# Performance work log

Measured on AMD Instinct MI355X. Metric: run time of the kernel, lower is better.

## Reference

```python
import jax, jax.numpy as jnp
import numpy as np

L, H, D, HS = 6, 8, 512, 64
EPS = 1e-5


def _ln(x, g, b):
    m = jnp.mean(x, -1, keepdims=True)
    v = jnp.mean((x - m) ** 2, -1, keepdims=True)
    return (x - m) * jax.lax.rsqrt(v + EPS) * g + b


def _posenc(T, C):
    pos = jnp.arange(T, dtype=jnp.float32)[:, None]
    div = jnp.exp(jnp.arange(0, C, 2, dtype=jnp.float32) * (-jnp.log(10000.0) / C))
    pe = jnp.zeros((T, C), jnp.float32)
    pe = pe.at[:, 0::2].set(jnp.sin(pos * div))
    pe = pe.at[:, 1::2].set(jnp.cos(pos * div))
    return pe


def setup_inputs() -> dict:
    B, T, F, V, E, O = 8, 1024, 32, 7, 16, 49
    key = jax.random.key(0)
    ks = jax.random.split(key, 16)
    s = 0.02
    inp = {
        'code': jax.random.randint(ks[0], (B, T, F), 0, V),
        'lengths': jax.random.randint(ks[1], (B,), T // 2, T + 1),
        'emb': s * jax.random.normal(ks[2], (V, E), jnp.float32),
        'Wq': s * jax.random.normal(ks[3], (L, H, D, HS), jnp.float32),
        'Wk': s * jax.random.normal(ks[4], (L, H, D, HS), jnp.float32),
        'Wv': s * jax.random.normal(ks[5], (L, H, D, HS), jnp.float32),
        'Wo': s * jax.random.normal(ks[6], (L, D, D), jnp.float32),
        'bo': jnp.zeros((L, D), jnp.float32),
        'W1': s * jax.random.normal(ks[7], (L, D, 4 * D), jnp.float32),
        'b1': jnp.zeros((L, 4 * D), jnp.float32),
        'W2': s * jax.random.normal(ks[8], (L, 4 * D, D), jnp.float32),
        'b2': jnp.zeros((L, D), jnp.float32),
        'ln1_g': jnp.ones((L, D), jnp.float32),
        'ln1_b': jnp.zeros((L, D), jnp.float32),
        'ln2_g': jnp.ones((L, D), jnp.float32),
        'ln2_b': jnp.zeros((L, D), jnp.float32),
        'lnf_g': jnp.ones((D,), jnp.float32),
        'lnf_b': jnp.zeros((D,), jnp.float32),
        'attn_w': s * jax.random.normal(ks[9], (D, 1), jnp.float32),
        'attn_b': jnp.zeros((1,), jnp.float32),
        'head_w': s * jax.random.normal(ks[10], (D, 49), jnp.float32),
        'head_b': jnp.zeros((49,), jnp.float32),
    }
    return inp


def reference(code, lengths, emb, Wq, Wk, Wv, Wo, bo, W1, b1, W2, b2,
              ln1_g, ln1_b, ln2_g, ln2_b, lnf_g, lnf_b,
              attn_w, attn_b, head_w, head_b):
    B, T, F = code.shape
    # token embedding (B,T,F,E) -> (B,T,D) plus sinusoidal positions
    x = emb[code].reshape(B, T, D) + _posenc(T, D)
    mask = jnp.arange(T) < lengths[:, None]          # (B,T) valid positions
    col_mask = mask[:, None, None, :]                # mask key columns
    row_mask = mask[:, None, :, None]                # zero padded query rows
    for l in range(L):
        xn = _ln(x, ln1_g[l], ln1_b[l])
        q = jnp.einsum('btd,hde->bhte', xn, Wq[l])
        k = jnp.einsum('btd,hde->bhte', xn, Wk[l])
        v = jnp.einsum('btd,hde->bhte', xn, Wv[l])
        wei = jnp.einsum('bhte,bhse->bhts', q, k) * (HS ** -0.5)
        wei = jnp.where(col_mask, wei, -jnp.inf)
        wei = jax.nn.softmax(wei, axis=-1)
        wei = jnp.where(row_mask, wei, 0.0)
        o = jnp.einsum('bhts,bhse->bthe', wei, v).reshape(B, T, H * HS)
        x = x + o @ Wo[l] + bo[l]
        xn = _ln(x, ln2_g[l], ln2_b[l])
        x = x + jax.nn.gelu(xn @ W1[l] + b1[l], approximate=False) @ W2[l] + b2[l]
    x = _ln(x, lnf_g, lnf_b)
    # attention pooling over time
    scores = x @ attn_w + attn_b                     # (B,T,1)
    scores = jnp.where(mask[:, :, None], scores, -jnp.inf)
    aw = jax.nn.softmax(scores, axis=1)
    summary = jnp.sum(aw * x, axis=1)                # (B,D)
    logits = summary @ head_w + head_b               # (B,49)
    return logits
```

## Files before the change

### kernel.cpp

```cpp
#include <hip/hip_runtime.h>
#include <math.h>

#define TT 1024
#define BB 8
#define DD 512
#define HH 8
#define HSZ 64
#define LL 6
#define FF4 2048

typedef __attribute__((ext_vector_type(8))) short short8;
typedef __attribute__((ext_vector_type(4))) float floatx4;
typedef unsigned short ushort_t;
typedef unsigned int uint_t;

__device__ __forceinline__ ushort_t f2bf(float f) {
  uint_t u = __float_as_uint(f);
  u += 0x7fff + ((u >> 16) & 1);
  return (ushort_t)(u >> 16);
}
__device__ __forceinline__ float bf2f(ushort_t h) {
  return __uint_as_float(((uint_t)h) << 16);
}

#if defined(__has_builtin)
#if __has_builtin(__builtin_amdgcn_sched_group_barrier)
#define SGB(mask, n) __builtin_amdgcn_sched_group_barrier(mask, n, 0)
#endif
#endif
#ifndef SGB
#define SGB(mask, n)
#endif


__global__ __launch_bounds__(256) void k_embed(const int* __restrict__ code,
                                               const float* __restrict__ emb,
                                               float* __restrict__ x,
                                               const int* __restrict__ lengths) {
  int idx = blockIdx.x * 256 + threadIdx.x;
  int c = idx & (DD - 1);
  int bt = idx >> 9;
  int t = bt & (TT - 1);
  if (t >= lengths[bt >> 10]) return;
  int f = c >> 4, e = c & 15;
  int vv = code[bt * 32 + f];
  int i = c >> 1;
  float freq = expf((float)(2 * i) * (-9.210340371976184f / 512.f));
  float ang = (float)t * freq;
  float pe = (c & 1) ? cosf(ang) : sinf(ang);
  x[idx] = emb[vv * 16 + e] + pe;
}

__global__ __launch_bounds__(256) void k_ln(const float* __restrict__ x,
                                            ushort_t* __restrict__ yB,
                                            float* __restrict__ yF,
                                            const float* __restrict__ g,
                                            const float* __restrict__ b,
                                            const float* __restrict__ aw,
                                            const float* __restrict__ ab,
                                            float* __restrict__ scores,
                                            const int* __restrict__ lengths) {
  int row0 = blockIdx.x * 4;
  if ((row0 & (TT - 1)) >= lengths[row0 >> 10]) return;
  int wave = threadIdx.x >> 6, lane = threadIdx.x & 63;
  int row = row0 + wave;
  const float* xr = x + (size_t)row * DD;
  float v[8];
  *(float4*)&v[0] = *(const float4*)(xr + lane * 8);
  *(float4*)&v[4] = *(const float4*)(xr + lane * 8 + 4);
  float s = 0.f;
#pragma unroll
  for (int j = 0; j < 8; ++j) s += v[j];
#pragma unroll
  for (int off = 32; off; off >>= 1) s += __shfl_down(s, off, 64);
  float mean = __shfl(s, 0, 64) * (1.f / DD);
  float qv = 0.f;
#pragma unroll
  for (int j = 0; j < 8; ++j) { float d = v[j] - mean; qv += d * d; }
#pragma unroll
  for (int off = 32; off; off >>= 1) qv += __shfl_down(qv, off, 64);
  float rs = rsqrtf(__shfl(qv, 0, 64) * (1.f / DD) + 1e-5f);
  float ov[8];
  float sdot = 0.f;
#pragma unroll
  for (int e = 0; e < 8; ++e) {
    int c = lane * 8 + e;
    ov[e] = (v[e] - mean) * rs * g[c] + b[c];
    if (scores) sdot += ov[e] * aw[c];
  }
  if (yB) {
    short8 o8;
#pragma unroll
    for (int e = 0; e < 8; ++e) o8[e] = (short)f2bf(ov[e]);
    size_t ad = (((size_t)(row >> 4) * 16 + (lane >> 2)) << 9) + ((lane & 3) * 16 + (row & 15)) * 8;
    *(short8*)(yB + ad) = o8;
  } else {
    float* yr = yF + (size_t)row * DD + lane * 8;
    *(float4*)yr = *(float4*)&ov[0];
    *(float4*)(yr + 4) = *(float4*)&ov[4];
  }
  if (scores) {
#pragma unroll
    for (int off = 32; off; off >>= 1) sdot += __shfl_down(sdot, off, 64);
    if (lane == 0) scores[row] = sdot + ab[0];
  }
}

__global__ __launch_bounds__(256) void k_packw(const float* __restrict__ in,
                                               ushort_t* __restrict__ out,
                                               int Nin, long in_ms, int nh,
                                               long os_l, int nblk, int Kout) {
  __shared__ float t4[64][65];
  int mz = blockIdx.z;
  const float* ip = in + (size_t)mz * in_ms;
  ushort_t* op = out + (size_t)(mz / nh) * os_l;
  int nbase = (mz % nh) * nblk + blockIdx.y * 64;
  int k0 = blockIdx.x * 64;
  int cc = threadIdx.x & 63, r0 = threadIdx.x >> 6;
#pragma unroll
  for (int i = 0; i < 16; ++i) {
    int r = r0 * 16 + i;
    t4[r][cc] = ip[(size_t)(k0 + r) * Nin + (nbase - (mz % nh) * nblk) + cc];
  }
  __syncthreads();
#pragma unroll
  for (int half = 0; half < 2; ++half) {
    int c = threadIdx.x + half * 256;
    int joct = c >> 6, nl = c & 63;
    int n = nbase + nl, k = k0 + joct * 8;
    short8 v8;
#pragma unroll
    for (int e = 0; e < 8; ++e) v8[e] = (short)f2bf(t4[joct * 8 + e][nl]);
    size_t ad = (((size_t)(n >> 4) * (Kout >> 5) + (k >> 5)) << 9) + (((k >> 3) & 3) * 16 + (n & 15)) * 8;
    *(short8*)(op + ad) = v8;
  }
}

template <int MT, int NT, int D>
__global__ __launch_bounds__(64, (MT == 4) ? 3 : 4) void k_pgemm(const ushort_t* __restrict__ Apk,
                                                                 const ushort_t* __restrict__ Bpk,
                                                                 const float* __restrict__ resid,
                                                                 const float* __restrict__ bias,
                                                                 float* __restrict__ outF,
                                                                 ushort_t* __restrict__ outB,
                                                                 int M, int N, int K, int mode,
                                                                 const int* __restrict__ lengths) {
  __shared__ ushort_t Cb[MT == 4 ? 64 * 80 : 64];
  const int lane = threadIdx.x;
  const int quad = lane >> 4, l16 = lane & 15;
  const int gx = N / (NT * 16);
  int id = blockIdx.x;
  int bx = (id >> 3) % gx;
  int by = (id / (8 * gx)) * 8 + (id & 7);
  const int row0 = by * (MT * 16), col0 = bx * (NT * 16);
  if (lengths && (row0 & (TT - 1)) >= lengths[row0 >> 10]) return;
  const int nk = K >> 5;
  const ushort_t* Ab = Apk + (((size_t)(row0 >> 4) * nk) << 9) + lane * 8;
  const ushort_t* Bb = Bpk + (((size_t)(col0 >> 4) * nk) << 9) + lane * 8;
  floatx4 acc[MT][NT] = {};
  short8 af[D][MT], bf[D][NT];
#pragma unroll
  for (int d = 0; d < D; ++d) {
#pragma unroll
    for (int mt = 0; mt < MT; ++mt) af[d][mt] = *(const short8*)(Ab + (((size_t)(mt * nk + d)) << 9));
#pragma unroll
    for (int nt = 0; nt < NT; ++nt) bf[d][nt] = *(const short8*)(Bb + (((size_t)(nt * nk + d)) << 9));
  }
  int kc = 0;
  for (; kc + D < nk; kc += D) {
#pragma unroll
    for (int d = 0; d < D; ++d) {
#pragma unroll
      for (int mt = 0; mt < MT; ++mt)
#pragma unroll
        for (int nt = 0; nt < NT; ++nt)
          acc[mt][nt] = __builtin_amdgcn_mfma_f32_16x16x32_bf16(af[d][mt], bf[d][nt], acc[mt][nt], 0, 0, 0);
      SGB(0x008, MT * NT);
      const int nxt = kc + d + D;
#pragma unroll
      for (int mt = 0; mt < MT; ++mt) af[d][mt] = *(const short8*)(Ab + (((size_t)(mt * nk + nxt)) << 9));
#pragma unroll
      for (int nt = 0; nt < NT; ++nt) bf[d][nt] = *(const short8*)(Bb + (((size_t)(nt * nk + nxt)) << 9));
      SGB(0x020, MT + NT);
    }
  }
#pragma unroll
  for (int d = 0; d < D; ++d)
#pragma unroll
    for (int mt = 0; mt < MT; ++mt)
#pragma unroll
      for (int nt = 0; nt < NT; ++nt)
        acc[mt][nt] = __builtin_amdgcn_mfma_f32_16x16x32_bf16(af[d][mt], bf[d][nt], acc[mt][nt], 0, 0, 0);

  if (MT == 4 && mode == 2) {
#pragma unroll
    for (int mt = 0; mt < MT; ++mt)
#pragma unroll
      for (int nt = 0; nt < NT; ++nt) {
        floatx4 a4 = acc[mt][nt];
#pragma unroll
        for (int r = 0; r < 4; ++r) {
          float val = a4[r] + bias[col0 + nt * 16 + l16];
          val = 0.5f * val * (1.f + erff(val * 0.7071067811865475f));
          Cb[(mt * 16 + quad * 4 + r) * 80 + nt * 16 + l16] = f2bf(val);
        }
      }
#pragma unroll
    for (int mt2 = 0; mt2 < 4; ++mt2)
#pragma unroll
      for (int kt2 = 0; kt2 < 2; ++kt2) {
        short8 v8 = *(const short8*)&Cb[(mt2 * 16 + l16) * 80 + kt2 * 32 + quad * 8];
        size_t ad = ((((size_t)(row0 >> 4) + mt2) * (N >> 5) + (col0 >> 5) + kt2) << 9) + lane * 8;
        *(short8*)(outB + ad) = v8;
      }
  } else {
    const float qscale = (mode == 3 && col0 < 512) ? 0.125f : 1.0f;
#pragma unroll
    for (int mt = 0; mt < MT; ++mt)
#pragma unroll
      for (int nt = 0; nt < NT; ++nt) {
        floatx4 a4 = acc[mt][nt];
#pragma unroll
        for (int r = 0; r < 4; ++r) {
          int row = row0 + mt * 16 + quad * 4 + r;
          int col = col0 + nt * 16 + l16;
          float val = a4[r];
          if (bias) val += bias[col];
          size_t idx = (size_t)row * N + col;
          if (mode == 1) outF[idx] = val + resid[idx];
          else outB[idx] = f2bf(val * qscale);
        }
      }
  }
}

__global__ __launch_bounds__(256) void k_attn(const ushort_t* __restrict__ qkv,
                                              const int* __restrict__ lengths,
                                              ushort_t* __restrict__ o) {
  __shared__ ushort_t Ks[64 * 72];
  __shared__ ushort_t Vt[64 * 72];
  __shared__ ushort_t Ps[4][16 * 72];
  const int tid = threadIdx.x;
  const int w = tid >> 6, lane = tid & 63;
  const int quad = lane >> 4, l16 = lane & 15;
  const int tile = blockIdx.x & 15;
  const int bh = blockIdx.x >> 4;
  const int b = bh >> 3, h = bh & 7;
  const int len = lengths[b];
  if (tile * 64 >= len) return;
  const int tqa = tile * 64 + w * 16 + l16;
  const ushort_t* qp = qkv + ((size_t)(b * TT + tqa)) * 1536 + h * HSZ + quad * 8;
  short8 qf0 = *(const short8*)qp;
  short8 qf1 = *(const short8*)(qp + 32);
  floatx4 oacc[4] = {};
  float lsum[4] = {0.f, 0.f, 0.f, 0.f};
  const int skey = tid >> 2, sseg = (tid & 3) << 4;
  const int vkp = (tid & 31) << 1, vds = (tid >> 5) << 3;
  const int nkt = (len + 63) >> 6;
  for (int kt = 0; kt < nkt; ++kt) {
    const int s0 = kt * 64;
    __syncthreads();
    {
      const ushort_t* kp = qkv + ((size_t)(b * TT + s0 + skey)) * 1536 + 512 + h * HSZ + sseg;
      short8 k0 = *(const short8*)kp;
      short8 k1 = *(const short8*)(kp + 8);
      *(short8*)&Ks[skey * 72 + sseg] = k0;
      *(short8*)&Ks[skey * 72 + sseg + 8] = k1;
      const ushort_t* vp0 = qkv + ((size_t)(b * TT + s0 + vkp)) * 1536 + 1024 + h * HSZ + vds;
      short8 v0 = *(const short8*)vp0;
      short8 v1 = *(const short8*)(vp0 + 1536);
#pragma unroll
      for (int i = 0; i < 8; ++i) {
        ushort2 pr;
        pr.x = (ushort_t)v0[i];
        pr.y = (ushort_t)v1[i];
        *(ushort2*)&Vt[(vds + i) * 72 + vkp] = pr;
      }
    }
    __syncthreads();
    floatx4 sacc[4] = {};
#pragma unroll
    for (int nt = 0; nt < 4; ++nt) {
      short8 kf0 = *(const short8*)&Ks[(nt * 16 + l16) * 72 + quad * 8];
      short8 kf1 = *(const short8*)&Ks[(nt * 16 + l16) * 72 + 32 + quad * 8];
      sacc[nt] = __builtin_amdgcn_mfma_f32_16x16x32_bf16(qf0, kf0, sacc[nt], 0, 0, 0);
      sacc[nt] = __builtin_amdgcn_mfma_f32_16x16x32_bf16(qf1, kf1, sacc[nt], 0, 0, 0);
    }
    float p[4][4];
    if (kt == nkt - 1) {
#pragma unroll
      for (int nt = 0; nt < 4; ++nt) {
        bool valid = (s0 + nt * 16 + l16 < len);
#pragma unroll
        for (int r = 0; r < 4; ++r) p[nt][r] = valid ? __expf(sacc[nt][r]) : 0.f;
      }
    } else {
#pragma unroll
      for (int nt = 0; nt < 4; ++nt)
#pragma unroll
        for (int r = 0; r < 4; ++r) p[nt][r] = __expf(sacc[nt][r]);
    }
#pragma unroll
    for (int r = 0; r < 4; ++r)
#pragma unroll
      for (int nt = 0; nt < 4; ++nt) {
        lsum[r] += p[nt][r];
        Ps[w][(quad * 4 + r) * 72 + nt * 16 + l16] = f2bf(p[nt][r]);
      }
    short8 pf0 = *(const short8*)&Ps[w][l16 * 72 + quad * 8];
    short8 pf1 = *(const short8*)&Ps[w][l16 * 72 + 32 + quad * 8];
#pragma unroll
    for (int nt = 0; nt < 4; ++nt) {
      short8 vf0 = *(const short8*)&Vt[(nt * 16 + l16) * 72 + quad * 8];
      short8 vf1 = *(const short8*)&Vt[(nt * 16 + l16) * 72 + 32 + quad * 8];
      oacc[nt] = __builtin_amdgcn_mfma_f32_16x16x32_bf16(pf0, vf0, oacc[nt], 0, 0, 0);
      oacc[nt] = __builtin_amdgcn_mfma_f32_16x16x32_bf16(pf1, vf1, oacc[nt], 0, 0, 0);
    }
  }
#pragma unroll
  for (int off = 1; off < 16; off <<= 1) {
#pragma unroll
    for (int r = 0; r < 4; ++r) lsum[r] += __shfl_xor(lsum[r], off, 64);
  }
#pragma unroll
  for (int r = 0; r < 4; ++r) {
    int t = tile * 64 + w * 16 + quad * 4 + r;
    float inv = (t < len) ? 1.f / lsum[r] : 0.f;
#pragma unroll
    for (int nt = 0; nt < 4; ++nt)
      Ps[w][(quad * 4 + r) * 72 + nt * 16 + l16] = f2bf(oacc[nt][r] * inv);
  }
  const int mtile = b * 64 + tile * 4 + w;
#pragma unroll
  for (int kt2 = 0; kt2 < 2; ++kt2) {
    short8 v8 = *(const short8*)&Ps[w][l16 * 72 + kt2 * 32 + quad * 8];
    size_t ad = (((size_t)mtile * 16 + h * 2 + kt2) << 9) + lane * 8;
    *(short8*)(o + ad) = v8;
  }
}

__global__ __launch_bounds__(256) void k_softw(const float* __restrict__ scores,
                                               const int* __restrict__ lengths,
                                               float* __restrict__ wts) {
  __shared__ float red[8];
  int tid = threadIdx.x, b = blockIdx.x;
  int len = lengths[b];
  const float* sb = scores + b * TT;
  float m = -1e30f;
  for (int t = tid; t < len; t += 256) m = fmaxf(m, sb[t]);
#pragma unroll
  for (int off = 32; off; off >>= 1) m = fmaxf(m, __shfl_down(m, off, 64));
  if ((tid & 63) == 0) red[tid >> 6] = m;
  __syncthreads();
  m = fmaxf(fmaxf(red[0], red[1]), fmaxf(red[2], red[3]));
  float ssum = 0.f;
  for (int t = tid; t < len; t += 256) ssum += __expf(sb[t] - m);
#pragma unroll
  for (int off = 32; off; off >>= 1) ssum += __shfl_down(ssum, off, 64);
  if ((tid & 63) == 0) red[4 + (tid >> 6)] = ssum;
  __syncthreads();
  float inv = 1.f / (red[4] + red[5] + red[6] + red[7]);
  for (int t = tid; t < TT; t += 256)
    wts[b * TT + t] = (t < len) ? __expf(sb[t] - m) * inv : 0.f;
}

__global__ __launch_bounds__(256) void k_wsum(const float* __restrict__ xf,
                                              const float* __restrict__ wts,
                                              float* __restrict__ partial,
                                              const int* __restrict__ lengths) {
  int b = blockIdx.x, c = blockIdx.y, tid = threadIdx.x;
  float* pp = partial + ((size_t)b * 16 + c) * DD;
  if (c * 64 >= lengths[b]) {
    pp[tid] = 0.f;
    pp[tid + 256] = 0.f;
    return;
  }
  const float* xb = xf + ((size_t)b * TT + c * 64) * DD;
  const float* wb = wts + b * TT + c * 64;
  float a0 = 0.f, a1 = 0.f;
  for (int t = 0; t < 64; ++t) {
    float wv = wb[t];
    a0 += wv * xb[(size_t)t * DD + tid];
    a1 += wv * xb[(size_t)t * DD + tid + 256];
  }
  pp[tid] = a0;
  pp[tid + 256] = a1;
}

__global__ __launch_bounds__(64) void k_head(const float* __restrict__ partial,
                                             const float* __restrict__ head_w,
                                             const float* __restrict__ head_b,
                                             float* __restrict__ out) {
  __shared__ float ssum[DD];
  int b = blockIdx.x, tid = threadIdx.x;
  for (int d = tid; d < DD; d += 64) {
    float s = 0.f;
#pragma unroll
    for (int c = 0; c < 16; ++c) s += partial[((size_t)b * 16 + c) * DD + d];
    ssum[d] = s;
  }
  __syncthreads();
  if (tid < 49) {
    float s = head_b[tid];
    for (int d = 0; d < DD; ++d) s += ssum[d] * head_w[d * 49 + tid];
    out[b * 49 + tid] = s;
  }
}

extern "C" void kernel_launch(void* const* d_in, const int* in_sizes, int n_in,
                              void* d_out, int out_size, void* d_ws, size_t ws_size,
                              hipStream_t stream) {
  const int* code = (const int*)d_in[0];
  const int* lengths = (const int*)d_in[1];
  const float* emb = (const float*)d_in[2];
  const float* Wq = (const float*)d_in[3];
  const float* Wk = (const float*)d_in[4];
  const float* Wv = (const float*)d_in[5];
  const float* Wo = (const float*)d_in[6];
  const float* bo = (const float*)d_in[7];
  const float* W1 = (const float*)d_in[8];
  const float* b1 = (const float*)d_in[9];
  const float* W2 = (const float*)d_in[10];
  const float* b2 = (const float*)d_in[11];
  const float* ln1_g = (const float*)d_in[12];
  const float* ln1_b = (const float*)d_in[13];
  const float* ln2_g = (const float*)d_in[14];
  const float* ln2_b = (const float*)d_in[15];
  const float* lnf_g = (const float*)d_in[16];
  const float* lnf_b = (const float*)d_in[17];
  const float* attn_w = (const float*)d_in[18];
  const float* attn_b = (const float*)d_in[19];
  const float* head_w = (const float*)d_in[20];
  const float* head_b = (const float*)d_in[21];
  float* out = (float*)d_out;

  const size_t NTOK = (size_t)BB * TT;
  float* x = (float*)d_ws;
  ushort_t* xn = (ushort_t*)(x + NTOK * DD);
  ushort_t* un = xn + NTOK * DD;
  ushort_t* qkv = un;
  ushort_t* h1 = un;
  float* xf = (float*)un;
  ushort_t* wqpk = un + (size_t)NTOK * FF4;
  ushort_t* wopk = wqpk + (size_t)LL * 1536 * 512;
  ushort_t* w1pk = wopk + (size_t)LL * 512 * 512;
  ushort_t* w2pk = w1pk + (size_t)LL * 512 * FF4;
  float* scores = (float*)(w2pk + (size_t)LL * FF4 * 512);
  float* wts = scores + NTOK;
  float* partial = wts + NTOK;

  k_packw<<<dim3(8, 1, 48), 256, 0, stream>>>(Wq, wqpk,              64, (long)512 * 64, 8, (long)1536 * 512, 64, 512);
  k_packw<<<dim3(8, 1, 48), 256, 0, stream>>>(Wk, wqpk + 512 * 512,  64, (long)512 * 64, 8, (long)1536 * 512, 64, 512);
  k_packw<<<dim3(8, 1, 48), 256, 0, stream>>>(Wv, wqpk + 1024 * 512, 64, (long)512 * 64, 8, (long)1536 * 512, 64, 512);
  k_packw<<<dim3(8, 8, 6), 256, 0, stream>>>(Wo, wopk, 512, (long)512 * 512, 1, (long)512 * 512, 0, 512);
  k_packw<<<dim3(8, 32, 6), 256, 0, stream>>>(W1, w1pk, 2048, (long)512 * 2048, 1, (long)2048 * 512, 0, 512);
  k_packw<<<dim3(32, 8, 6), 256, 0, stream>>>(W2, w2pk, 512, (long)2048 * 512, 1, (long)512 * 2048, 0, 2048);

  k_embed<<<dim3((unsigned)((NTOK * DD) / 256)), dim3(256), 0, stream>>>(code, emb, x, lengths);

  for (int l = 0; l < LL; ++l) {
    k_ln<<<dim3(NTOK / 4), 256, 0, stream>>>(x, xn, nullptr, ln1_g + l * DD, ln1_b + l * DD,
                                             nullptr, nullptr, nullptr, lengths);
    k_pgemm<4, 4, 2><<<dim3(24 * 128), 64, 0, stream>>>(xn, wqpk + (size_t)l * 1536 * 512, nullptr, nullptr,
                                                        nullptr, qkv, (int)NTOK, 1536, 512, 3, lengths);
    k_attn<<<dim3(BB * HH * (TT / 64)), 256, 0, stream>>>(qkv, lengths, xn);
    k_pgemm<2, 2, 4><<<dim3(16 * 256), 64, 0, stream>>>(xn, wopk + (size_t)l * 512 * 512, x, bo + l * DD,
                                                        x, nullptr, (int)NTOK, 512, 512, 1, lengths);
    k_ln<<<dim3(NTOK / 4), 256, 0, stream>>>(x, xn, nullptr, ln2_g + l * DD, ln2_b + l * DD,
                                             nullptr, nullptr, nullptr, lengths);
    k_pgemm<4, 4, 2><<<dim3(32 * 128), 64, 0, stream>>>(xn, w1pk + (size_t)l * 512 * FF4, nullptr, b1 + l * FF4,
                                                        nullptr, h1, (int)NTOK, FF4, 512, 2, lengths);
    k_pgemm<2, 2, 4><<<dim3(16 * 256), 64, 0, stream>>>(h1, w2pk + (size_t)l * FF4 * 512, x, b2 + l * DD,
                                                        x, nullptr, (int)NTOK, 512, 2048, 1, lengths);
  }
  k_ln<<<dim3(NTOK / 4), 256, 0, stream>>>(x, nullptr, xf, lnf_g, lnf_b,
                                           attn_w, attn_b, scores, lengths);
  k_softw<<<dim3(BB), 256, 0, stream>>>(scores, lengths, wts);
  k_wsum<<<dim3(BB, 16), 256, 0, stream>>>(xf, wts, partial, lengths);
  k_head<<<dim3(BB), 64, 0, stream>>>(partial, head_w, head_b, out);
}
```

Baseline: 1.350 ms.

## Replace register-prefetch single-wave GEMM with 4-wave LDS double-buffered tiled GEMM

```diff
diff --git a/kernel.cpp b/kernel.cpp
--- a/kernel.cpp
+++ b/kernel.cpp
@@ -22,15 +22,6 @@
 __device__ __forceinline__ float bf2f(ushort_t h) {
   return __uint_as_float(((uint_t)h) << 16);
 }
-
-#if defined(__has_builtin)
-#if __has_builtin(__builtin_amdgcn_sched_group_barrier)
-#define SGB(mask, n) __builtin_amdgcn_sched_group_barrier(mask, n, 0)
-#endif
-#endif
-#ifndef SGB
-#define SGB(mask, n)
-#endif
 
 
 __global__ __launch_bounds__(256) void k_embed(const int* __restrict__ code,
@@ -136,63 +127,97 @@
   }
 }
 
-template <int MT, int NT, int D>
-__global__ __launch_bounds__(64, (MT == 4) ? 3 : 4) void k_pgemm(const ushort_t* __restrict__ Apk,
-                                                                 const ushort_t* __restrict__ Bpk,
-                                                                 const float* __restrict__ resid,
-                                                                 const float* __restrict__ bias,
-                                                                 float* __restrict__ outF,
-                                                                 ushort_t* __restrict__ outB,
-                                                                 int M, int N, int K, int mode,
-                                                                 const int* __restrict__ lengths) {
-  __shared__ ushort_t Cb[MT == 4 ? 64 * 80 : 64];
-  const int lane = threadIdx.x;
+template <int BN>
+__global__ __launch_bounds__(256, 3) void k_sgemm(const ushort_t* __restrict__ Apk,
+                                                  const ushort_t* __restrict__ Bpk,
+                                                  const float* __restrict__ resid,
+                                                  const float* __restrict__ bias,
+                                                  float* __restrict__ outF,
+                                                  ushort_t* __restrict__ outB,
+                                                  int M, int N, int K, int mode,
+                                                  const int* __restrict__ lengths) {
+  constexpr int MT = (BN == 128) ? 4 : 2;
+  constexpr int NT = 4;
+  constexpr int NA = 8;
+  constexpr int NB = BN / 16;
+  constexpr int NFRAG = NA + NB;
+  constexpr int NF = NFRAG / 4;
+  constexpr int BUFU = NFRAG * 512;
+  __shared__ ushort_t lds[(BN == 128) ? 20480 : 2 * BUFU];
+
+  const int tid = threadIdx.x;
+  const int w = tid >> 6, lane = tid & 63;
   const int quad = lane >> 4, l16 = lane & 15;
-  const int gx = N / (NT * 16);
+  const int gx = N / BN;
   int id = blockIdx.x;
   int bx = (id >> 3) % gx;
   int by = (id / (8 * gx)) * 8 + (id & 7);
-  const int row0 = by * (MT * 16), col0 = bx * (NT * 16);
+  const int row0 = by * 128, col0 = bx * BN;
   if (lengths && (row0 & (TT - 1)) >= lengths[row0 >> 10]) return;
   const int nk = K >> 5;
-  const ushort_t* Ab = Apk + (((size_t)(row0 >> 4) * nk) << 9) + lane * 8;
-  const ushort_t* Bb = Bpk + (((size_t)(col0 >> 4) * nk) << 9) + lane * 8;
+
+  const int wrow0 = (BN == 128) ? row0 + (w >> 1) * 64 : row0 + w * 32;
+  const int wcol0 = (BN == 128) ? col0 + (w & 1) * 64 : col0;
+  const int ar16 = (wrow0 - row0) >> 4;
+  const int bc16 = NA + ((wcol0 - col0) >> 4);
+
+  const ushort_t* gbase[NF];
+#pragma unroll
+  for (int i = 0; i < NF; ++i) {
+    int f = w * NF + i;
+    if (f < NA)
+      gbase[i] = Apk + (((size_t)((row0 >> 4) + f) * nk) << 9) + lane * 8;
+    else
+      gbase[i] = Bpk + (((size_t)((col0 >> 4) + (f - NA)) * nk) << 9) + lane * 8;
+  }
+  const int ldst = (w * NF) * 512 + lane * 8;
+
   floatx4 acc[MT][NT] = {};
-  short8 af[D][MT], bf[D][NT];
-#pragma unroll
-  for (int d = 0; d < D; ++d) {
-#pragma unroll
-    for (int mt = 0; mt < MT; ++mt) af[d][mt] = *(const short8*)(Ab + (((size_t)(mt * nk + d)) << 9));
-#pragma unroll
-    for (int nt = 0; nt < NT; ++nt) bf[d][nt] = *(const short8*)(Bb + (((size_t)(nt * nk + d)) << 9));
-  }
-  int kc = 0;
-  for (; kc + D < nk; kc += D) {
-#pragma unroll
-    for (int d = 0; d < D; ++d) {
-#pragma unroll
-      for (int mt = 0; mt < MT; ++mt)
-#pragma unroll
-        for (int nt = 0; nt < NT; ++nt)
-          acc[mt][nt] = __builtin_amdgcn_mfma_f32_16x16x32_bf16(af[d][mt], bf[d][nt], acc[mt][nt], 0, 0, 0);
-      SGB(0x008, MT * NT);
-      const int nxt = kc + d + D;
-#pragma unroll
-      for (int mt = 0; mt < MT; ++mt) af[d][mt] = *(const short8*)(Ab + (((size_t)(mt * nk + nxt)) << 9));
-#pragma unroll
-      for (int nt = 0; nt < NT; ++nt) bf[d][nt] = *(const short8*)(Bb + (((size_t)(nt * nk + nxt)) << 9));
-      SGB(0x020, MT + NT);
-    }
-  }
-#pragma unroll
-  for (int d = 0; d < D; ++d)
+  short8 greg[NF];
+
+#pragma unroll
+  for (int i = 0; i < NF; ++i) greg[i] = *(const short8*)(gbase[i]);
+#pragma unroll
+  for (int i = 0; i < NF; ++i) *(short8*)&lds[ldst + i * 512] = greg[i];
+  __syncthreads();
+
+  int bufo = 0;
+  for (int kc = 0; kc + 1 < nk; ++kc) {
+#pragma unroll
+    for (int i = 0; i < NF; ++i)
+      greg[i] = *(const short8*)(gbase[i] + ((size_t)(kc + 1) << 9));
+    short8 af[MT], bfv[NT];
+#pragma unroll
+    for (int mt = 0; mt < MT; ++mt) af[mt] = *(const short8*)&lds[bufo + (ar16 + mt) * 512 + lane * 8];
+#pragma unroll
+    for (int nt = 0; nt < NT; ++nt) bfv[nt] = *(const short8*)&lds[bufo + (bc16 + nt) * 512 + lane * 8];
 #pragma unroll
     for (int mt = 0; mt < MT; ++mt)
 #pragma unroll
       for (int nt = 0; nt < NT; ++nt)
-        acc[mt][nt] = __builtin_amdgcn_mfma_f32_16x16x32_bf16(af[d][mt], bf[d][nt], acc[mt][nt], 0, 0, 0);
-
-  if (MT == 4 && mode == 2) {
+        acc[mt][nt] = __builtin_amdgcn_mfma_f32_16x16x32_bf16(af[mt], bfv[nt], acc[mt][nt], 0, 0, 0);
+    const int nbufo = bufo ^ BUFU;
+#pragma unroll
+    for (int i = 0; i < NF; ++i) *(short8*)&lds[nbufo + ldst + i * 512] = greg[i];
+    __syncthreads();
+    bufo = nbufo;
+  }
+  {
+    short8 af[MT], bfv[NT];
+#pragma unroll
+    for (int mt = 0; mt < MT; ++mt) af[mt] = *(const short8*)&lds[bufo + (ar16 + mt) * 512 + lane * 8];
+#pragma unroll
+    for (int nt = 0; nt < NT; ++nt) bfv[nt] = *(const short8*)&lds[bufo + (bc16 + nt) * 512 + lane * 8];
+#pragma unroll
+    for (int mt = 0; mt < MT; ++mt)
+#pragma unroll
+      for (int nt = 0; nt < NT; ++nt)
+        acc[mt][nt] = __builtin_amdgcn_mfma_f32_16x16x32_bf16(af[mt], bfv[nt], acc[mt][nt], 0, 0, 0);
+  }
+
+  if (BN == 128 && mode == 2) {
+    __syncthreads();
+    ushort_t* Cb = &lds[w * 5120];
 #pragma unroll
     for (int mt = 0; mt < MT; ++mt)
 #pragma unroll
@@ -200,7 +225,7 @@
         floatx4 a4 = acc[mt][nt];
 #pragma unroll
         for (int r = 0; r < 4; ++r) {
-          float val = a4[r] + bias[col0 + nt * 16 + l16];
+          float val = a4[r] + bias[wcol0 + nt * 16 + l16];
           val = 0.5f * val * (1.f + erff(val * 0.7071067811865475f));
           Cb[(mt * 16 + quad * 4 + r) * 80 + nt * 16 + l16] = f2bf(val);
         }
@@ -210,7 +235,7 @@
 #pragma unroll
       for (int kt2 = 0; kt2 < 2; ++kt2) {
         short8 v8 = *(const short8*)&Cb[(mt2 * 16 + l16) * 80 + kt2 * 32 + quad * 8];
-        size_t ad = ((((size_t)(row0 >> 4) + mt2) * (N >> 5) + (col0 >> 5) + kt2) << 9) + lane * 8;
+        size_t ad = ((((size_t)(wrow0 >> 4) + mt2) * (N >> 5) + (wcol0 >> 5) + kt2) << 9) + lane * 8;
         *(short8*)(outB + ad) = v8;
       }
   } else {
@@ -222,8 +247,8 @@
         floatx4 a4 = acc[mt][nt];
 #pragma unroll
         for (int r = 0; r < 4; ++r) {
-          int row = row0 + mt * 16 + quad * 4 + r;
-          int col = col0 + nt * 16 + l16;
+          int row = wrow0 + mt * 16 + quad * 4 + r;
+          int col = wcol0 + nt * 16 + l16;
           float val = a4[r];
           if (bias) val += bias[col];
           size_t idx = (size_t)row * N + col;
@@ -461,17 +486,17 @@
   for (int l = 0; l < LL; ++l) {
     k_ln<<<dim3(NTOK / 4), 256, 0, stream>>>(x, xn, nullptr, ln1_g + l * DD, ln1_b + l * DD,
                                              nullptr, nullptr, nullptr, lengths);
-    k_pgemm<4, 4, 2><<<dim3(24 * 128), 64, 0, stream>>>(xn, wqpk + (size_t)l * 1536 * 512, nullptr, nullptr,
-                                                        nullptr, qkv, (int)NTOK, 1536, 512, 3, lengths);
+    k_sgemm<128><<<dim3(768), 256, 0, stream>>>(xn, wqpk + (size_t)l * 1536 * 512, nullptr, nullptr,
+                                                nullptr, qkv, (int)NTOK, 1536, 512, 3, lengths);
     k_attn<<<dim3(BB * HH * (TT / 64)), 256, 0, stream>>>(qkv, lengths, xn);
-    k_pgemm<2, 2, 4><<<dim3(16 * 256), 64, 0, stream>>>(xn, wopk + (size_t)l * 512 * 512, x, bo + l * DD,
-                                                        x, nullptr, (int)NTOK, 512, 512, 1, lengths);
+    k_sgemm<64><<<dim3(512), 256, 0, stream>>>(xn, wopk + (size_t)l * 512 * 512, x, bo + l * DD,
+                                               x, nullptr, (int)NTOK, 512, 512, 1, lengths);
     k_ln<<<dim3(NTOK / 4), 256, 0, stream>>>(x, xn, nullptr, ln2_g + l * DD, ln2_b + l * DD,
                                              nullptr, nullptr, nullptr, lengths);
-    k_pgemm<4, 4, 2><<<dim3(32 * 128), 64, 0, stream>>>(xn, w1pk + (size_t)l * 512 * FF4, nullptr, b1 + l * FF4,
-                                                        nullptr, h1, (int)NTOK, FF4, 512, 2, lengths);
-    k_pgemm<2, 2, 4><<<dim3(16 * 256), 64, 0, stream>>>(h1, w2pk + (size_t)l * FF4 * 512, x, b2 + l * DD,
-                                                        x, nullptr, (int)NTOK, 512, 2048, 1, lengths);
+    k_sgemm<128><<<dim3(1024), 256, 0, stream>>>(xn, w1pk + (size_t)l * 512 * FF4, nullptr, b1 + l * FF4,
+                                                 nullptr, h1, (int)NTOK, FF4, 512, 2, lengths);
+    k_sgemm<64><<<dim3(512), 256, 0, stream>>>(h1, w2pk + (size_t)l * FF4 * 512, x, b2 + l * DD,
+                                               x, nullptr, (int)NTOK, 512, 2048, 1, lengths);
   }
   k_ln<<<dim3(NTOK / 4), 256, 0, stream>>>(x, nullptr, xf, lnf_g, lnf_b,
                                            attn_w, attn_b, scores, lengths);
```

Result: slower. 1.394 ms (+3.2%).
